# Kernel tuning notes

Hardware: AMD Instinct MI355X
Metric: run time of the kernel (lower is better)

The kernel has to match this reference:

```python
import jax, jax.numpy as jnp
import numpy as np

NUM_HEADS = 4
NUM_LEVELS = 4
NUM_POINTS = 8
EMBED = 256
HEAD_DIM = EMBED // NUM_HEADS
SHAPES = np.array([[92, 160], [46, 80], [23, 40], [12, 20]], dtype=np.int64)  # (h, w) per level
NUM_VALUE = int((SHAPES[:, 0] * SHAPES[:, 1]).sum())  # 19560
DEPTH = 64
NQ = 20000
BS = 1
NZ = 4  # num_Z_anchors; NUM_POINTS % NZ == 0


def _depth_bias():
    # replicates init_smpl_off_weights for sampling_offsets_depth.bias
    th = np.arange(NUM_HEADS) * (2.0 * np.pi / NUM_HEADS)
    g = ((np.cos(th) + np.sin(th)) / 2.0)[:, None, None] * np.ones((NUM_HEADS, NUM_LEVELS, NUM_POINTS))
    g = g * (np.arange(NUM_POINTS) + 1)[None, None, :]
    return jnp.asarray(g.reshape(-1), dtype=jnp.float32)


def setup_inputs() -> dict:
    key = jax.random.key(0)
    ks = jax.random.split(key, 8)
    f = jnp.float32
    s = 0.02
    query = jax.random.normal(ks[0], (BS, NQ, EMBED), f)
    value = jax.random.normal(ks[1], (BS, NUM_VALUE, EMBED), f)
    value_dpt_dist = jax.nn.softmax(jax.random.normal(ks[2], (BS, NUM_VALUE, DEPTH), f), axis=-1)
    reference_points = jax.random.uniform(ks[3], (BS, NQ, NZ, 3), f)
    spatial_shapes = jnp.asarray(SHAPES)
    level_start_index = jnp.asarray(np.concatenate([[0], np.cumsum(SHAPES[:, 0] * SHAPES[:, 1])[:-1]]))
    Wv = jax.random.normal(ks[4], (EMBED, EMBED), f) * s
    bv = jnp.zeros((EMBED,), f)
    Wo = jax.random.normal(ks[5], (EMBED, NUM_HEADS * NUM_LEVELS * NUM_POINTS * 2), f) * s
    bo = jax.random.normal(ks[6], (NUM_HEADS * NUM_LEVELS * NUM_POINTS * 2,), f) * 0.5
    Wod = jnp.zeros((EMBED, NUM_HEADS * NUM_LEVELS * NUM_POINTS), f)  # constant_init 0.0
    bod = _depth_bias()
    Wa = jax.random.normal(ks[7], (EMBED, NUM_HEADS * NUM_LEVELS * NUM_POINTS), f) * s
    ba = jnp.zeros((NUM_HEADS * NUM_LEVELS * NUM_POINTS,), f)
    return dict(query=query, value=value, value_dpt_dist=value_dpt_dist,
                reference_points=reference_points, spatial_shapes=spatial_shapes,
                level_start_index=level_start_index, Wv=Wv, bv=bv, Wo=Wo, bo=bo,
                Wod=Wod, bod=bod, Wa=Wa, ba=ba)


def _forward(query, value, value_dpt_dist, reference_points, spatial_shapes,
             level_start_index, Wv, bv, Wo, bo, Wod, bod, Wa, ba):
    bs, nq, _ = query.shape
    H, L, P = NUM_HEADS, NUM_LEVELS, NUM_POINTS
    dh = HEAD_DIM
    D = value_dpt_dist.shape[-1]
    dt = query.dtype
    shapes = np.asarray(spatial_shapes)  # static level shapes

    v = (value @ Wv + bv).reshape(bs, -1, H, dh)  # value_proj
    off_uv = (query @ Wo + bo).reshape(bs, nq, H, L, P, 2)
    off_d = (query @ Wod + bod).reshape(bs, nq, H, L, P, 1)
    off = jnp.concatenate([off_uv, off_d], axis=-1)  # (bs,nq,H,L,P,3)
    attn = jax.nn.softmax((query @ Wa + ba).reshape(bs, nq, H, L * P), axis=-1)
    attn = attn.reshape(bs, nq, H, L, P)

    # offset_normalizer = (w, h, D) per level
    norm = jnp.asarray(np.stack([shapes[:, 1], shapes[:, 0], np.full(L, D)], -1), dtype=dt)
    off = off / norm[None, None, None, :, None, :]
    Z = reference_points.shape[2]
    off = off.reshape(bs, nq, H, L, P // Z, Z, 3)
    loc = (reference_points[:, :, None, None, None, :, :] + off).reshape(bs, nq, H, L, P, 3)

    starts = np.concatenate([[0], np.cumsum(shapes[:, 0] * shapes[:, 1])]).astype(int)
    gather_bh = jax.vmap(jax.vmap(lambda a, i: a[i]))   # over (bs, heads)
    gather_b = jax.vmap(lambda a, i: a[i])              # over bs

    out = jnp.zeros((bs, nq, H, dh), dt)
    for l in range(L):
        Hl, Wl = int(shapes[l, 0]), int(shapes[l, 1])
        v_l = v[:, starts[l]:starts[l + 1]].transpose(0, 2, 1, 3)          # (bs,H,HW,dh)
        d_l = value_dpt_dist[:, starts[l]:starts[l + 1]].reshape(bs, Hl * Wl * D)
        ll = loc[:, :, :, l]                                               # (bs,nq,H,P,3)
        # grid_sample (align_corners=False) pixel coordinates
        x = ll[..., 0] * Wl - 0.5
        y = ll[..., 1] * Hl - 0.5
        z = ll[..., 2] * D - 0.5
        x0f, y0f, z0f = jnp.floor(x), jnp.floor(y), jnp.floor(z)
        fx, fy, fz = x - x0f, y - y0f, z - z0f
        x0 = x0f.astype(jnp.int32); y0 = y0f.astype(jnp.int32); z0 = z0f.astype(jnp.int32)
        z0c = jnp.clip(z0, 0, D - 1)
        z1c = jnp.clip(z0 + 1, 0, D - 1)
        wz0 = (1.0 - fz) * ((z0 >= 0) & (z0 <= D - 1)).astype(dt)
        wz1 = fz * ((z0 + 1 >= 0) & (z0 + 1 <= D - 1)).astype(dt)

        acc = jnp.zeros((bs, nq, H, P, dh), dt)
        for xi, wx in ((x0, 1.0 - fx), (x0 + 1, fx)):
            for yi, wy in ((y0, 1.0 - fy), (y0 + 1, fy)):
                valid = ((xi >= 0) & (xi < Wl) & (yi >= 0) & (yi < Hl)).astype(dt)
                w_uv = wx * wy * valid                                     # (bs,nq,H,P)
                idx = jnp.clip(yi, 0, Hl - 1) * Wl + jnp.clip(xi, 0, Wl - 1)
                idx_h = idx.transpose(0, 2, 1, 3).reshape(bs, H, nq * P)
                val = gather_bh(v_l, idx_h).reshape(bs, H, nq, P, dh).transpose(0, 2, 1, 3, 4)
                d0 = gather_b(d_l, (idx * D + z0c).reshape(bs, -1)).reshape(bs, nq, H, P)
                d1 = gather_b(d_l, (idx * D + z1c).reshape(bs, -1)).reshape(bs, nq, H, P)
                dscore = wz0 * d0 + wz1 * d1                               # depth lerp at this spatial corner
                acc = acc + (w_uv * dscore)[..., None] * val
        out = out + jnp.einsum('bqhp,bqhpd->bqhd', attn[:, :, :, l], acc)
    return out.reshape(bs, nq, H * dh)


def reference(query, value, value_dpt_dist, reference_points, spatial_shapes,
              level_start_index, Wv, bv, Wo, bo, Wod, bod, Wa, ba):
    return _forward(query, value, value_dpt_dist, reference_points, spatial_shapes,
                    level_start_index, Wv, bv, Wo, bo, Wod, bod, Wa, ba)
```

## Files before the change

kernel.cpp:

```cpp
#include <hip/hip_runtime.h>
#include <math.h>

#define NQ    20000
#define NV    19560
#define NHEAD 4
#define DEPTHD 64

typedef __attribute__((ext_vector_type(8))) short short8;
typedef __attribute__((ext_vector_type(4))) float f32x4;

__device__ __forceinline__ ushort f2bf(float f) {
    uint32_t u = __float_as_uint(f);
    uint32_t r = (u + 0x7FFFu + ((u >> 16) & 1u)) >> 16;
    return (ushort)r;
}
__device__ __forceinline__ float bf_lo(uint32_t d) { return __uint_as_float(d << 16); }
__device__ __forceinline__ float bf_hi(uint32_t d) { return __uint_as_float(d & 0xFFFF0000u); }

__global__ __launch_bounds__(256) void prep_weights(
    const float* __restrict__ Wv, const float* __restrict__ Wo,
    const float* __restrict__ Wod, const float* __restrict__ Wa,
    const float* __restrict__ bo, const float* __restrict__ bod,
    const float* __restrict__ ba,
    ushort* __restrict__ WvT, ushort* __restrict__ WqT, float* __restrict__ bq)
{
    const int b = blockIdx.x;
    const int k = threadIdx.x;
    if (b < 256) {
        WvT[b * 256 + k] = f2bf(Wv[k * 256 + b]);
    } else if (b < 768) {
        const int n = b - 256;
        float w;
        if (n < 256)      w = Wo [k * 256 + n];
        else if (n < 384) w = Wod[k * 128 + (n - 256)];
        else              w = Wa [k * 128 + (n - 384)];
        WqT[n * 256 + k] = f2bf(w);
    } else {
        for (int i = k; i < 512; i += 256) {
            float v;
            if (i < 256)      v = bo[i];
            else if (i < 384) v = bod[i - 256];
            else              v = ba[i - 384];
            bq[i] = v;
        }
    }
}

template<bool BF16_OUT>
__global__ __launch_bounds__(256) void gemm_mfma_bf16(
    const float* __restrict__ A, const ushort* __restrict__ BT,
    const float* __restrict__ bias, void* __restrict__ Cout,
    int M, int ldc)
{
    constexpr int K = 256, BK = 32;
    __shared__ ushort Asb[128][40];
    __shared__ ushort Bsb[128][40];

    const int tid  = threadIdx.x;
    const int lane = tid & 63;
    const int wave = tid >> 6;
    const int wm   = wave >> 1;
    const int wn   = wave & 1;
    const int brow = blockIdx.y * 128;
    const int bcol = blockIdx.x * 128;
    const int l15  = lane & 15;
    const int kg   = lane >> 4;

    f32x4 acc[4][4] = {};

    const int rA    = tid >> 1;
    const int partA = tid & 1;

    for (int k0 = 0; k0 < K; k0 += BK) {
        {
            ushort tmp[16];
            if (brow + rA < M) {
                const float* ap = A + (size_t)(brow + rA) * K + k0 + partA * 16;
                #pragma unroll
                for (int i = 0; i < 4; ++i) {
                    float4 v = *reinterpret_cast<const float4*>(ap + i * 4);
                    tmp[i * 4 + 0] = f2bf(v.x);
                    tmp[i * 4 + 1] = f2bf(v.y);
                    tmp[i * 4 + 2] = f2bf(v.z);
                    tmp[i * 4 + 3] = f2bf(v.w);
                }
            } else {
                #pragma unroll
                for (int i = 0; i < 16; ++i) tmp[i] = 0;
            }
            *reinterpret_cast<uint4*>(&Asb[rA][partA * 16 + 0]) = *reinterpret_cast<uint4*>(tmp);
            *reinterpret_cast<uint4*>(&Asb[rA][partA * 16 + 8]) = *reinterpret_cast<uint4*>(tmp + 8);
        }
        #pragma unroll
        for (int i = 0; i < 2; ++i) {
            int f  = tid + i * 256;
            int n  = f >> 2;
            int c8 = (f & 3) * 8;
            uint4 v = *reinterpret_cast<const uint4*>(BT + (size_t)(bcol + n) * K + k0 + c8);
            *reinterpret_cast<uint4*>(&Bsb[n][c8]) = v;
        }
        __syncthreads();

        short8 af[4], bfv[4];
        #pragma unroll
        for (int mf = 0; mf < 4; ++mf)
            af[mf] = *reinterpret_cast<const short8*>(&Asb[wm * 64 + mf * 16 + l15][kg * 8]);
        #pragma unroll
        for (int nf = 0; nf < 4; ++nf)
            bfv[nf] = *reinterpret_cast<const short8*>(&Bsb[wn * 64 + nf * 16 + l15][kg * 8]);
        #pragma unroll
        for (int mf = 0; mf < 4; ++mf)
            #pragma unroll
            for (int nf = 0; nf < 4; ++nf)
                acc[mf][nf] = __builtin_amdgcn_mfma_f32_16x16x32_bf16(af[mf], bfv[nf], acc[mf][nf], 0, 0, 0);
        __syncthreads();
    }

    #pragma unroll
    for (int mf = 0; mf < 4; ++mf) {
        #pragma unroll
        for (int reg = 0; reg < 4; ++reg) {
            int row = brow + wm * 64 + mf * 16 + kg * 4 + reg;
            if (row >= M) continue;
            #pragma unroll
            for (int nf = 0; nf < 4; ++nf) {
                int col = bcol + wn * 64 + nf * 16 + l15;
                float v = acc[mf][nf][reg] + bias[col];
                if (BF16_OUT)
                    ((ushort*)Cout)[(size_t)row * ldc + col] = f2bf(v);
                else
                    ((float*)Cout)[(size_t)row * ldc + col] = v;
            }
        }
    }
}

__global__ __launch_bounds__(256) void deform_sample(
    const float* __restrict__ qproj,
    const ushort* __restrict__ vproj,
    const float* __restrict__ ddist,
    const float* __restrict__ refpts,
    float* __restrict__ out)
{
    const int q    = blockIdx.x;
    const int h    = threadIdx.x >> 6;
    const int lane = threadIdx.x & 63;
    const int j    = lane & 31;

    __shared__ float2 sm[NHEAD][128];

    const float* qrow = qproj + (size_t)q * 512;

    float logit = qrow[384 + h * 32 + j];
    float m = logit;
    #pragma unroll
    for (int o = 16; o; o >>= 1) m = fmaxf(m, __shfl_xor(m, o));
    float e = __expf(logit - m);
    float s = e;
    #pragma unroll
    for (int o = 16; o; o >>= 1) s += __shfl_xor(s, o);
    const float aw = e / s;

    const int l  = j >> 3;
    const int p  = j & 7;
    const int zi = p & 3;
    const int Wl = 160 >> l;
    const int Hl = (l == 0) ? 92 : (l == 1) ? 46 : (l == 2) ? 23 : 12;
    const int st = (l == 0) ? 0  : (l == 1) ? 14720 : (l == 2) ? 18400 : 19320;

    const int oidx = (h * 4 + l) * 8 + p;
    const float ox = qrow[oidx * 2 + 0];
    const float oy = qrow[oidx * 2 + 1];
    const float od = qrow[256 + oidx];
    const float rx = refpts[(q * 4 + zi) * 3 + 0];
    const float ry = refpts[(q * 4 + zi) * 3 + 1];
    const float rz = refpts[(q * 4 + zi) * 3 + 2];

    const float x = fmaf(rx, (float)Wl, ox - 0.5f);
    const float y = fmaf(ry, (float)Hl, oy - 0.5f);
    const float z = fmaf(rz, 64.0f,     od - 0.5f);
    const float x0f = floorf(x), y0f = floorf(y), z0f = floorf(z);
    const float fx = x - x0f, fy = y - y0f, fz = z - z0f;
    const int x0 = (int)x0f, y0 = (int)y0f, z0 = (int)z0f;

    const int z0c = min(max(z0, 0), DEPTHD - 1);
    const int z1c = min(max(z0 + 1, 0), DEPTHD - 1);
    const float wz0 = (z0 >= 0 && z0 <= DEPTHD - 1) ? (1.f - fz) : 0.f;
    const float wz1 = (z0 >= -1 && z0 <= DEPTHD - 2) ? fz : 0.f;

    #pragma unroll
    for (int c = 0; c < 4; ++c) {
        const int   cy = c >> 1, cx = c & 1;
        const int   yi = y0 + cy, xi = x0 + cx;
        const float wy = cy ? fy : (1.f - fy);
        const float wx = cx ? fx : (1.f - fx);
        const bool  valid = (xi >= 0) & (xi < Wl) & (yi >= 0) & (yi < Hl);
        const int   yc = min(max(yi, 0), Hl - 1);
        const int   xc = min(max(xi, 0), Wl - 1);
        const int   row = st + yc * Wl + xc;
        const float* dptr = ddist + (size_t)row * 64;
        const float dscore = wz0 * dptr[z0c] + wz1 * dptr[z1c];
        const float coef = valid ? (aw * wx * wy * dscore) : 0.f;
        if (lane < 32)
            sm[h][c * 32 + j] = make_float2(coef, __int_as_float(row * 512 + h * 128));
    }
    __syncthreads();

    const int g   = lane >> 3;
    const int ch8 = (lane & 7) << 3;
    const uint32_t chb = (uint32_t)(ch8 << 1);
    const char* vb = (const char*)vproj;
    const float2* smh = sm[h];

    float acc[8] = {};
    #pragma unroll 8
    for (int t = 0; t < 16; ++t) {
        const float2 wi = smh[t * 8 + g];
        const uint32_t off = (uint32_t)__float_as_int(wi.y) + chb;
        const uint4 raw = *reinterpret_cast<const uint4*>(vb + off);
        const float w = wi.x;
        acc[0] = fmaf(w, bf_lo(raw.x), acc[0]);
        acc[1] = fmaf(w, bf_hi(raw.x), acc[1]);
        acc[2] = fmaf(w, bf_lo(raw.y), acc[2]);
        acc[3] = fmaf(w, bf_hi(raw.y), acc[3]);
        acc[4] = fmaf(w, bf_lo(raw.z), acc[4]);
        acc[5] = fmaf(w, bf_hi(raw.z), acc[5]);
        acc[6] = fmaf(w, bf_lo(raw.w), acc[6]);
        acc[7] = fmaf(w, bf_hi(raw.w), acc[7]);
    }

    #pragma unroll
    for (int o = 8; o <= 32; o <<= 1)
        #pragma unroll
        for (int k = 0; k < 8; ++k)
            acc[k] += __shfl_xor(acc[k], o);

    if (g == 0) {
        float* op = out + (size_t)q * 256 + h * 64 + ch8;
        float4 o0 = make_float4(acc[0], acc[1], acc[2], acc[3]);
        float4 o1 = make_float4(acc[4], acc[5], acc[6], acc[7]);
        *reinterpret_cast<float4*>(op)     = o0;
        *reinterpret_cast<float4*>(op + 4) = o1;
    }
}

extern "C" void kernel_launch(void* const* d_in, const int* in_sizes, int n_in,
                              void* d_out, int out_size, void* d_ws, size_t ws_size,
                              hipStream_t stream)
{
    const float* query  = (const float*)d_in[0];
    const float* value  = (const float*)d_in[1];
    const float* ddist  = (const float*)d_in[2];
    const float* refpts = (const float*)d_in[3];
    const float* Wv  = (const float*)d_in[6];
    const float* bv  = (const float*)d_in[7];
    const float* Wo  = (const float*)d_in[8];
    const float* bo  = (const float*)d_in[9];
    const float* Wod = (const float*)d_in[10];
    const float* bod = (const float*)d_in[11];
    const float* Wa  = (const float*)d_in[12];
    const float* ba  = (const float*)d_in[13];
    float* out = (float*)d_out;

    char* ws = (char*)d_ws;
    ushort* vbuf = (ushort*)ws;
    float*  qbuf = (float*)(ws + 10014720);
    ushort* WvT  = (ushort*)(ws + 10014720 + 40960000);
    ushort* WqT  = WvT + 256 * 256;
    float*  bq   = (float*)(WqT + 512 * 256);

    dim3 blk(256);

    prep_weights<<<dim3(769), blk, 0, stream>>>(Wv, Wo, Wod, Wa, bo, bod, ba, WvT, WqT, bq);

    gemm_mfma_bf16<true><<<dim3(2, (NV + 127) / 128), blk, 0, stream>>>(
        value, WvT, bv, vbuf, NV, 256);

    gemm_mfma_bf16<false><<<dim3(4, (NQ + 127) / 128), blk, 0, stream>>>(
        query, WqT, bq, qbuf, NQ, 512);

    deform_sample<<<dim3(NQ), blk, 0, stream>>>(qbuf, vbuf, ddist, refpts, out);
}
```

Before: 168.7 us.

## Pack depth pairs as bf16 and process two queries per sampling block

Adds a prep kernel that packs each depth value and its next neighbour as a bf16 pair, so each spatial corner needs one 32-bit gather instead of two fp32 gathers. The sampling kernel now handles two queries per block, using both half-waves for coefficient setup, and drops the block barrier. Two independent value gathers per iteration give more memory parallelism. In exchange it adds an extra pass over the 5MB depth tensor, lowers depth precision to bf16, and raises register pressure from the doubled accumulators. The barrier removal relies on each wave writing and reading only its own shared-memory slice.

```diff
diff --git a/kernel.cpp b/kernel.cpp
--- a/kernel.cpp
+++ b/kernel.cpp
@@ -44,6 +44,17 @@
             bq[i] = v;
         }
     }
+}
+
+__global__ __launch_bounds__(256) void prep_ddist(
+    const float* __restrict__ ddist, uint32_t* __restrict__ ddist2)
+{
+    const int idx = blockIdx.x * 256 + threadIdx.x;
+    if (idx >= NV * 64) return;
+    const int z = idx & 63;
+    const float lo = ddist[idx];
+    const float hi = ddist[idx + ((z < 63) ? 1 : 0)];
+    ddist2[idx] = (uint32_t)f2bf(lo) | ((uint32_t)f2bf(hi) << 16);
 }
 
 template<bool BF16_OUT>
@@ -138,16 +149,18 @@
 __global__ __launch_bounds__(256) void deform_sample(
     const float* __restrict__ qproj,
     const ushort* __restrict__ vproj,
-    const float* __restrict__ ddist,
+    const uint32_t* __restrict__ ddist2,
     const float* __restrict__ refpts,
     float* __restrict__ out)
 {
-    const int q    = blockIdx.x;
+    const int b    = blockIdx.x;
     const int h    = threadIdx.x >> 6;
     const int lane = threadIdx.x & 63;
     const int j    = lane & 31;
-
-    __shared__ float2 sm[NHEAD][128];
+    const int qq   = lane >> 5;
+    const int q    = 2 * b + qq;
+
+    __shared__ float2 sm[NHEAD][2][128];
 
     const float* qrow = qproj + (size_t)q * 512;
 
@@ -184,9 +197,8 @@
     const int x0 = (int)x0f, y0 = (int)y0f, z0 = (int)z0f;
 
     const int z0c = min(max(z0, 0), DEPTHD - 1);
-    const int z1c = min(max(z0 + 1, 0), DEPTHD - 1);
-    const float wz0 = (z0 >= 0 && z0 <= DEPTHD - 1) ? (1.f - fz) : 0.f;
-    const float wz1 = (z0 >= -1 && z0 <= DEPTHD - 2) ? fz : 0.f;
+    const float wlo = (z0 >= 0 && z0 <= 63) ? (1.f - fz) : ((z0 == -1) ? fz : 0.f);
+    const float whi = (z0 >= 0 && z0 <= 62) ? fz : 0.f;
 
     #pragma unroll
     for (int c = 0; c < 4; ++c) {
@@ -198,49 +210,60 @@
         const int   yc = min(max(yi, 0), Hl - 1);
         const int   xc = min(max(xi, 0), Wl - 1);
         const int   row = st + yc * Wl + xc;
-        const float* dptr = ddist + (size_t)row * 64;
-        const float dscore = wz0 * dptr[z0c] + wz1 * dptr[z1c];
+        const uint32_t pd = ddist2[row * 64 + z0c];
+        const float dscore = wlo * bf_lo(pd) + whi * bf_hi(pd);
         const float coef = valid ? (aw * wx * wy * dscore) : 0.f;
-        if (lane < 32)
-            sm[h][c * 32 + j] = make_float2(coef, __int_as_float(row * 512 + h * 128));
-    }
-    __syncthreads();
+        sm[h][qq][c * 32 + j] = make_float2(coef, __int_as_float(row * 512 + h * 128));
+    }
 
     const int g   = lane >> 3;
     const int ch8 = (lane & 7) << 3;
     const uint32_t chb = (uint32_t)(ch8 << 1);
     const char* vb = (const char*)vproj;
-    const float2* smh = sm[h];
-
-    float acc[8] = {};
-    #pragma unroll 8
+    const float2* s0 = sm[h][0];
+    const float2* s1 = sm[h][1];
+
+    float acc0[8] = {}, acc1[8] = {};
+    #pragma unroll
     for (int t = 0; t < 16; ++t) {
-        const float2 wi = smh[t * 8 + g];
-        const uint32_t off = (uint32_t)__float_as_int(wi.y) + chb;
-        const uint4 raw = *reinterpret_cast<const uint4*>(vb + off);
-        const float w = wi.x;
-        acc[0] = fmaf(w, bf_lo(raw.x), acc[0]);
-        acc[1] = fmaf(w, bf_hi(raw.x), acc[1]);
-        acc[2] = fmaf(w, bf_lo(raw.y), acc[2]);
-        acc[3] = fmaf(w, bf_hi(raw.y), acc[3]);
-        acc[4] = fmaf(w, bf_lo(raw.z), acc[4]);
-        acc[5] = fmaf(w, bf_hi(raw.z), acc[5]);
-        acc[6] = fmaf(w, bf_lo(raw.w), acc[6]);
-        acc[7] = fmaf(w, bf_hi(raw.w), acc[7]);
-    }
-
-    #pragma unroll
-    for (int o = 8; o <= 32; o <<= 1)
-        #pragma unroll
-        for (int k = 0; k < 8; ++k)
-            acc[k] += __shfl_xor(acc[k], o);
+        const float2 w0 = s0[t * 8 + g];
+        const float2 w1 = s1[t * 8 + g];
+        const uint4 r0 = *reinterpret_cast<const uint4*>(vb + ((uint32_t)__float_as_int(w0.y) + chb));
+        const uint4 r1 = *reinterpret_cast<const uint4*>(vb + ((uint32_t)__float_as_int(w1.y) + chb));
+        acc0[0] = fmaf(w0.x, bf_lo(r0.x), acc0[0]);
+        acc0[1] = fmaf(w0.x, bf_hi(r0.x), acc0[1]);
+        acc0[2] = fmaf(w0.x, bf_lo(r0.y), acc0[2]);
+        acc0[3] = fmaf(w0.x, bf_hi(r0.y), acc0[3]);
+        acc0[4] = fmaf(w0.x, bf_lo(r0.z), acc0[4]);
+        acc0[5] = fmaf(w0.x, bf_hi(r0.z), acc0[5]);
+        acc0[6] = fmaf(w0.x, bf_lo(r0.w), acc0[6]);
+        acc0[7] = fmaf(w0.x, bf_hi(r0.w), acc0[7]);
+        acc1[0] = fmaf(w1.x, bf_lo(r1.x), acc1[0]);
+        acc1[1] = fmaf(w1.x, bf_hi(r1.x), acc1[1]);
+        acc1[2] = fmaf(w1.x, bf_lo(r1.y), acc1[2]);
+        acc1[3] = fmaf(w1.x, bf_hi(r1.y), acc1[3]);
+        acc1[4] = fmaf(w1.x, bf_lo(r1.z), acc1[4]);
+        acc1[5] = fmaf(w1.x, bf_hi(r1.z), acc1[5]);
+        acc1[6] = fmaf(w1.x, bf_lo(r1.w), acc1[6]);
+        acc1[7] = fmaf(w1.x, bf_hi(r1.w), acc1[7]);
+    }
+
+    #pragma unroll
+    for (int o = 8; o <= 32; o <<= 1) {
+        #pragma unroll
+        for (int k = 0; k < 8; ++k) {
+            acc0[k] += __shfl_xor(acc0[k], o);
+            acc1[k] += __shfl_xor(acc1[k], o);
+        }
+    }
 
     if (g == 0) {
-        float* op = out + (size_t)q * 256 + h * 64 + ch8;
-        float4 o0 = make_float4(acc[0], acc[1], acc[2], acc[3]);
-        float4 o1 = make_float4(acc[4], acc[5], acc[6], acc[7]);
-        *reinterpret_cast<float4*>(op)     = o0;
-        *reinterpret_cast<float4*>(op + 4) = o1;
+        float* op0 = out + (size_t)(2 * b) * 256 + h * 64 + ch8;
+        *reinterpret_cast<float4*>(op0)     = make_float4(acc0[0], acc0[1], acc0[2], acc0[3]);
+        *reinterpret_cast<float4*>(op0 + 4) = make_float4(acc0[4], acc0[5], acc0[6], acc0[7]);
+        float* op1 = op0 + 256;
+        *reinterpret_cast<float4*>(op1)     = make_float4(acc1[0], acc1[1], acc1[2], acc1[3]);
+        *reinterpret_cast<float4*>(op1 + 4) = make_float4(acc1[4], acc1[5], acc1[6], acc1[7]);
     }
 }
 
@@ -263,15 +286,17 @@
     float* out = (float*)d_out;
 
     char* ws = (char*)d_ws;
-    ushort* vbuf = (ushort*)ws;
-    float*  qbuf = (float*)(ws + 10014720);
-    ushort* WvT  = (ushort*)(ws + 10014720 + 40960000);
-    ushort* WqT  = WvT + 256 * 256;
-    float*  bq   = (float*)(WqT + 512 * 256);
+    ushort*   vbuf   = (ushort*)ws;
+    float*    qbuf   = (float*)(ws + 10014720);
+    ushort*   WvT    = (ushort*)(ws + 10014720 + 40960000);
+    ushort*   WqT    = WvT + 256 * 256;
+    float*    bq     = (float*)(WqT + 512 * 256);
+    uint32_t* ddist2 = (uint32_t*)((char*)bq + 2048);
 
     dim3 blk(256);
 
     prep_weights<<<dim3(769), blk, 0, stream>>>(Wv, Wo, Wod, Wa, bo, bod, ba, WvT, WqT, bq);
+    prep_ddist<<<dim3((NV * 64 + 255) / 256), blk, 0, stream>>>(ddist, ddist2);
 
     gemm_mfma_bf16<true><<<dim3(2, (NV + 127) / 128), blk, 0, stream>>>(
         value, WvT, bv, vbuf, NV, 256);
@@ -279,5 +304,5 @@
     gemm_mfma_bf16<false><<<dim3(4, (NQ + 127) / 128), blk, 0, stream>>>(
         query, WqT, bq, qbuf, NQ, 512);
 
-    deform_sample<<<dim3(NQ), blk, 0, stream>>>(qbuf, vbuf, ddist, refpts, out);
-}
+    deform_sample<<<dim3(NQ / 2), blk, 0, stream>>>(qbuf, vbuf, ddist2, refpts, out);
+}
```

New measurement: 156.6 us. -7.1%, faster.
